# Performance work log

Measured on AMD Instinct MI355X. Metric: run time of the kernel, lower is better.

The kernel has to match this reference:

```python
import jax, jax.numpy as jnp
import numpy as np

N = 100000      # nodes
E = 800000      # edges (avg degree 8)
D_IN = 256      # input feature dim
D_H = 256       # hidden dim (hard-coded in module)
D_OUT = 128     # h_feats


def setup_inputs() -> dict:
    key = jax.random.key(0)
    ks = jax.random.split(key, 8)
    feat = jax.random.normal(ks[0], (N, D_IN), jnp.float32)
    src = jax.random.randint(ks[1], (E,), 0, N, dtype=jnp.int32)
    dst = jax.random.randint(ks[2], (E,), 0, N, dtype=jnp.int32)
    def lin(k, din, dout):
        return jax.random.normal(k, (din, dout), jnp.float32) / np.float32(np.sqrt(din))
    return {
        'feat': feat, 'src': src, 'dst': dst,
        'w_self1': lin(ks[3], D_IN, D_H), 'w_neigh1': lin(ks[4], D_IN, D_H),
        'b1': jnp.zeros((D_H,), jnp.float32),
        'w_self2': lin(ks[5], D_H, D_OUT), 'w_neigh2': lin(ks[6], D_H, D_OUT),
        'b2': jnp.zeros((D_OUT,), jnp.float32),
    }


def _sage_mean(h, src, dst, w_self, w_neigh, b):
    # DGL SAGEConv 'mean': rst = h @ W_self + mean_{in-neighbors}(h) @ W_neigh + b
    ones = jnp.ones((src.shape[0],), h.dtype)
    deg = jax.ops.segment_sum(ones, dst, num_segments=N)          # in-degree per node
    msum = jax.ops.segment_sum(h[src], dst, num_segments=N)      # [N, d] gather-scatter
    mean = msum / jnp.maximum(deg, 1.0)[:, None]                  # zero-degree -> 0
    return h @ w_self + mean @ w_neigh + b


def reference(feat, src, dst, w_self1, w_neigh1, b1, w_self2, w_neigh2, b2):
    h = jax.nn.relu(_sage_mean(feat, src, dst, w_self1, w_neigh1, b1))
    h = jax.nn.relu(_sage_mean(h, src, dst, w_self2, w_neigh2, b2))
    # F.normalize(h, dim=1): x / max(||x||_2, eps)
    norm = jnp.linalg.norm(h, axis=1, keepdims=True)
    return h / jnp.maximum(norm, 1e-12)
```

## Files before the change

kernel.cpp:

```cpp
#include <hip/hip_runtime.h>

#define DIN 256
#define DH  256
#define DOUT 128

typedef __attribute__((ext_vector_type(8))) short bf16x8;
typedef __attribute__((ext_vector_type(4))) float f32x4;
typedef __attribute__((ext_vector_type(2))) float f32x2;
typedef __attribute__((ext_vector_type(4))) unsigned short ushort4v;
typedef __attribute__((ext_vector_type(8))) unsigned short ushort8v;
typedef __attribute__((ext_vector_type(4))) unsigned int uint4v;

static __device__ __forceinline__ unsigned short f2bf(float x) {
    unsigned u = __float_as_uint(x);
    u += 0x7fffu + ((u >> 16) & 1u);
    return (unsigned short)(u >> 16);
}
static __device__ __forceinline__ float bf2f(unsigned short h) {
    return __uint_as_float(((unsigned)h) << 16);
}

static __device__ __forceinline__ void gload16(const unsigned short* g, void* l) {
    __builtin_amdgcn_global_load_lds(
        (const __attribute__((address_space(1))) unsigned int*)g,
        (__attribute__((address_space(3))) unsigned int*)l,
        16, 0, 0);
}

__global__ void count_kernel(const int* __restrict__ dst, int* __restrict__ cnt, int E) {
    int e = blockIdx.x * 256 + threadIdx.x;
    if (e < E) atomicAdd(&cnt[dst[e]], 1);
}

__global__ void block_sums_kernel(const int* __restrict__ cnt, int* __restrict__ partial, int N) {
    __shared__ int sdata[256];
    int t = threadIdx.x;
    int base = blockIdx.x * 1024;
    int s = 0;
#pragma unroll
    for (int j = 0; j < 4; ++j) {
        int i = base + t * 4 + j;
        if (i < N) s += cnt[i];
    }
    sdata[t] = s; __syncthreads();
    for (int o = 128; o; o >>= 1) {
        if (t < o) sdata[t] += sdata[t + o];
        __syncthreads();
    }
    if (t == 0) partial[blockIdx.x] = sdata[0];
}

__global__ void scan_block_kernel(int* __restrict__ cnt, const int* __restrict__ partial,
                                  int* __restrict__ off, int N, int E, int nb) {
    __shared__ int sdata[256];
    __shared__ int pbase;
    int b = blockIdx.x, t = threadIdx.x;

    int pv = (t < nb) ? partial[t] : 0;
    sdata[t] = pv; __syncthreads();
    for (int o = 1; o < 256; o <<= 1) {
        int y = (t >= o) ? sdata[t - o] : 0;
        __syncthreads();
        sdata[t] += y;
        __syncthreads();
    }
    if (t == 0) pbase = (b == 0) ? 0 : sdata[b - 1];
    __syncthreads();
    int base0 = pbase;
    __syncthreads();

    int base = b * 1024;
    int vals[4]; int local = 0;
#pragma unroll
    for (int j = 0; j < 4; ++j) {
        int i = base + t * 4 + j;
        vals[j] = (i < N) ? cnt[i] : 0;
        local += vals[j];
    }
    sdata[t] = local; __syncthreads();
    for (int o = 1; o < 256; o <<= 1) {
        int y = (t >= o) ? sdata[t - o] : 0;
        __syncthreads();
        sdata[t] += y;
        __syncthreads();
    }
    int run = sdata[t] - local + base0;
#pragma unroll
    for (int j = 0; j < 4; ++j) {
        int i = base + t * 4 + j;
        if (i < N) { off[i] = run; cnt[i] = run; }
        run += vals[j];
    }
    if (b == 0 && t == 0) off[N] = E;
}

__global__ void fillprep_kernel(const int* __restrict__ src, const int* __restrict__ dst,
                                int* __restrict__ cursor, int* __restrict__ csr, int E,
                                const float* __restrict__ feat, unsigned short* __restrict__ featb,
                                unsigned int* __restrict__ feat8, long long ncHalf,
                                const float* __restrict__ w_self1, const float* __restrict__ w_neigh1,
                                const float* __restrict__ w_self2, const float* __restrict__ w_neigh2,
                                unsigned short* __restrict__ ws1t, unsigned short* __restrict__ wn1t,
                                unsigned short* __restrict__ wcat,
                                int bFill, int bWt) {
    int b = blockIdx.x;
    if (b < bFill) {
        int e = b * 256 + threadIdx.x;
        if (e < E) {
            int d = dst[e];
            int p = atomicAdd(&cursor[d], 1);
            csr[p] = src[e];
        }
    } else if (b < bFill + bWt) {
        int idx = (b - bFill) * 256 + threadIdx.x;
        if (idx < 65536) {
            int nn = idx >> 8, k = idx & 255;
            ws1t[idx] = f2bf(w_self1[k * 256 + nn]);
        } else if (idx < 131072) {
            int j = idx - 65536; int nn = j >> 8, k = j & 255;
            wn1t[j] = f2bf(w_neigh1[k * 256 + nn]);
        } else if (idx < 163840) {
            int j = idx - 131072; int nn = j >> 8, k = j & 255;
            wcat[j] = f2bf(w_neigh2[k * 128 + nn]);
        } else if (idx < 196608) {
            int j = idx - 163840; int nn = j >> 8, k = j & 255;
            wcat[32768 + j] = f2bf(w_self2[k * 128 + nn]);
        }
    } else {
        long long i = (b - bFill - bWt) * 256LL + threadIdx.x;
        if (i >= ncHalf) return;
        long long i2 = i + ncHalf;
        f32x4 v0 = __builtin_nontemporal_load((const f32x4*)feat + i);
        f32x4 v1 = __builtin_nontemporal_load((const f32x4*)feat + i2);
        ushort4v o0, o1;
        o0[0] = f2bf(v0[0]); o0[1] = f2bf(v0[1]); o0[2] = f2bf(v0[2]); o0[3] = f2bf(v0[3]);
        o1[0] = f2bf(v1[0]); o1[1] = f2bf(v1[1]); o1[2] = f2bf(v1[2]); o1[3] = f2bf(v1[3]);
        *((ushort4v*)featb + i)  = o0;
        *((ushort4v*)featb + i2) = o1;
        int u0 = __builtin_amdgcn_cvt_pk_fp8_f32(v0[0], v0[1], 0, 0);
        u0     = __builtin_amdgcn_cvt_pk_fp8_f32(v0[2], v0[3], u0, 1);
        int u1 = __builtin_amdgcn_cvt_pk_fp8_f32(v1[0], v1[1], 0, 0);
        u1     = __builtin_amdgcn_cvt_pk_fp8_f32(v1[2], v1[3], u1, 1);
        feat8[i]  = (unsigned)u0;
        feat8[i2] = (unsigned)u1;
    }
}

__global__ void gather_mean256_kernel(const unsigned int* __restrict__ feat8, const int* __restrict__ off,
                                      const int* __restrict__ csr, unsigned short* __restrict__ agg, int N) {
    int wid  = (int)((blockIdx.x * (long long)blockDim.x + threadIdx.x) >> 6);
    int lane = threadIdx.x & 63;
    if (wid >= N) return;
    int start = off[wid], end = off[wid + 1];
    const int g   = lane >> 4;
    const int cl  = lane & 15;
    float a[16] = {};
    int e = start;
    for (; e + 7 < end; e += 8) {
        int s0 = csr[e + g], s1 = csr[e + 4 + g];
        uint4v v0 = *(const uint4v*)(feat8 + (long long)s0 * 64 + cl * 4);
        uint4v v1 = *(const uint4v*)(feat8 + (long long)s1 * 64 + cl * 4);
#pragma unroll
        for (int d = 0; d < 4; ++d) {
            f32x2 p0 = __builtin_amdgcn_cvt_pk_f32_fp8((int)v0[d], false);
            f32x2 p1 = __builtin_amdgcn_cvt_pk_f32_fp8((int)v0[d], true);
            f32x2 q0 = __builtin_amdgcn_cvt_pk_f32_fp8((int)v1[d], false);
            f32x2 q1 = __builtin_amdgcn_cvt_pk_f32_fp8((int)v1[d], true);
            a[d * 4 + 0] += p0[0] + q0[0];
            a[d * 4 + 1] += p0[1] + q0[1];
            a[d * 4 + 2] += p1[0] + q1[0];
            a[d * 4 + 3] += p1[1] + q1[1];
        }
    }
    for (; e < end; e += 4) {
        int idx = e + g;
        if (idx < end) {
            int s = csr[idx];
            uint4v v = *(const uint4v*)(feat8 + (long long)s * 64 + cl * 4);
#pragma unroll
            for (int d = 0; d < 4; ++d) {
                f32x2 p0 = __builtin_amdgcn_cvt_pk_f32_fp8((int)v[d], false);
                f32x2 p1 = __builtin_amdgcn_cvt_pk_f32_fp8((int)v[d], true);
                a[d * 4 + 0] += p0[0];
                a[d * 4 + 1] += p0[1];
                a[d * 4 + 2] += p1[0];
                a[d * 4 + 3] += p1[1];
            }
        }
    }
#pragma unroll
    for (int j = 0; j < 16; ++j) {
        a[j] += __shfl_xor(a[j], 16);
        a[j] += __shfl_xor(a[j], 32);
    }
    if (g == 0) {
        float inv = 1.0f / (float)max(end - start, 1);
        ushort8v o0, o1;
#pragma unroll
        for (int j = 0; j < 8; ++j) { o0[j] = f2bf(a[j] * inv); o1[j] = f2bf(a[8 + j] * inv); }
        unsigned short* dstp = agg + (long long)wid * 256 + cl * 16;
        *(ushort8v*)dstp       = o0;
        *(ushort8v*)(dstp + 8) = o1;
    }
}

__global__ __launch_bounds__(512)
void gemm1_kernel(const unsigned short* __restrict__ A,  const unsigned short* __restrict__ WT,
                  const unsigned short* __restrict__ A2, const unsigned short* __restrict__ WT2,
                  const float* __restrict__ bias, unsigned short* __restrict__ C, int M)
{
    const int K = 256;
    __shared__ __align__(16) char lds[2][24576];

    const int tid = threadIdx.x;
    const int wid = tid >> 6, lane = tid & 63;
    const int l15 = lane & 15, lg = lane >> 4;
    const int wr = wid >> 2, wc = wid & 3;
    const int row0 = blockIdx.x * 128;

    long long asrc; int adst;
    {
        int c = tid, r = c >> 2, s = c & 3;
        int kc = s ^ ((r >> 1) & 3);
        asrc = (long long)min(row0 + r, M - 1) * K + kc * 8;
        adst = c * 16;
    }
    long long bsrc[2]; int bdst[2];
#pragma unroll
    for (int i = 0; i < 2; ++i) {
        int c = wid * 128 + i * 64 + lane, r = c >> 2, s = c & 3;
        int kc = s ^ ((r >> 1) & 3);
        bsrc[i] = (long long)r * K + kc * 8;
        bdst[i] = 8192 + c * 16;
    }

    const int slot = (lg ^ ((l15 >> 1) & 3)) * 16;
    int aoff[4], boff[4];
#pragma unroll
    for (int m = 0; m < 4; ++m) aoff[m] = (wr * 64 + m * 16 + l15) * 64 + slot;
#pragma unroll
    for (int n = 0; n < 4; ++n) boff[n] = 8192 + (wc * 64 + n * 16 + l15) * 64 + slot;

    f32x4 acc[4][4] = {};

    auto stage = [&](int buf, int t) {
        const unsigned short* Ap = (t >= 8) ? A2 : A;
        const unsigned short* Wp = (t >= 8) ? WT2 : WT;
        int k0 = (t & 7) * 32;
        gload16(Ap + asrc + k0, &lds[buf][adst]);
        gload16(Wp + bsrc[0] + k0, &lds[buf][bdst[0]]);
        gload16(Wp + bsrc[1] + k0, &lds[buf][bdst[1]]);
    };

    stage(0, 0);
    __syncthreads();

    for (int t = 0; t < 16; ++t) {
        const int cur = t & 1;
        if (t + 1 < 16) stage(cur ^ 1, t + 1);
        const char* L = lds[cur];
        bf16x8 af[4], bfr[4];
#pragma unroll
        for (int m = 0; m < 4; ++m) af[m]  = *(const bf16x8*)(L + aoff[m]);
#pragma unroll
        for (int n = 0; n < 4; ++n) bfr[n] = *(const bf16x8*)(L + boff[n]);
#pragma unroll
        for (int m = 0; m < 4; ++m)
#pragma unroll
            for (int n = 0; n < 4; ++n)
                acc[m][n] = __builtin_amdgcn_mfma_f32_16x16x32_bf16(af[m], bfr[n], acc[m][n], 0, 0, 0);
        __syncthreads();
    }

#pragma unroll
    for (int m = 0; m < 4; ++m) {
#pragma unroll
        for (int rr = 0; rr < 4; ++rr) {
            int grow = row0 + wr * 64 + m * 16 + lg * 4 + rr;
            if (grow >= M) continue;
#pragma unroll
            for (int n = 0; n < 4; ++n) {
                int gcol = wc * 64 + n * 16 + l15;
                float v = fmaxf(acc[m][n][rr] + bias[gcol], 0.f);
                C[(long long)grow * 256 + gcol] = f2bf(v);
            }
        }
    }
}

__global__ __launch_bounds__(512)
void gemm23_kernel(const unsigned short* __restrict__ A, const unsigned short* __restrict__ WT,
                   const float* __restrict__ b2,
                   unsigned short* __restrict__ p2, unsigned short* __restrict__ self2, int M)
{
    const int K = 256;
    __shared__ __align__(16) char lds[2][24576];

    const int tid = threadIdx.x;
    const int wid = tid >> 6, lane = tid & 63;
    const int l15 = lane & 15, lg = lane >> 4;
    const int wr = wid >> 2, wc = wid & 3;
    const int row0 = blockIdx.x * 128;

    long long asrc; int adst;
    {
        int c = tid, r = c >> 2, s = c & 3;
        int kc = s ^ ((r >> 1) & 3);
        asrc = (long long)min(row0 + r, M - 1) * K + kc * 8;
        adst = c * 16;
    }
    long long bsrc[2]; int bdst[2];
#pragma unroll
    for (int i = 0; i < 2; ++i) {
        int c = wid * 128 + i * 64 + lane, r = c >> 2, s = c & 3;
        int kc = s ^ ((r >> 1) & 3);
        bsrc[i] = (long long)r * K + kc * 8;
        bdst[i] = 8192 + c * 16;
    }

    const int slot = (lg ^ ((l15 >> 1) & 3)) * 16;
    int aoff[4], boff[4];
#pragma unroll
    for (int m = 0; m < 4; ++m) aoff[m] = (wr * 64 + m * 16 + l15) * 64 + slot;
#pragma unroll
    for (int n = 0; n < 4; ++n) boff[n] = 8192 + (wc * 64 + n * 16 + l15) * 64 + slot;

    f32x4 acc[4][4] = {};

    auto stage = [&](int buf, int t) {
        int k0 = t * 32;
        gload16(A  + asrc + k0, &lds[buf][adst]);
        gload16(WT + bsrc[0] + k0, &lds[buf][bdst[0]]);
        gload16(WT + bsrc[1] + k0, &lds[buf][bdst[1]]);
    };

    stage(0, 0);
    __syncthreads();

    for (int t = 0; t < 8; ++t) {
        const int cur = t & 1;
        if (t + 1 < 8) stage(cur ^ 1, t + 1);
        const char* L = lds[cur];
        bf16x8 af[4], bfr[4];
#pragma unroll
        for (int m = 0; m < 4; ++m) af[m]  = *(const bf16x8*)(L + aoff[m]);
#pragma unroll
        for (int n = 0; n < 4; ++n) bfr[n] = *(const bf16x8*)(L + boff[n]);
#pragma unroll
        for (int m = 0; m < 4; ++m)
#pragma unroll
            for (int n = 0; n < 4; ++n)
                acc[m][n] = __builtin_amdgcn_mfma_f32_16x16x32_bf16(af[m], bfr[n], acc[m][n], 0, 0, 0);
        __syncthreads();
    }

    if (wc < 2) {
#pragma unroll
        for (int m = 0; m < 4; ++m)
#pragma unroll
            for (int rr = 0; rr < 4; ++rr) {
                int grow = row0 + wr * 64 + m * 16 + lg * 4 + rr;
                if (grow >= M) continue;
#pragma unroll
                for (int n = 0; n < 4; ++n) {
                    int col = wc * 64 + n * 16 + l15;
                    p2[(long long)grow * 128 + col] = f2bf(acc[m][n][rr]);
                }
            }
    } else {
        float bv[4];
#pragma unroll
        for (int n = 0; n < 4; ++n) bv[n] = b2[(wc - 2) * 64 + n * 16 + l15];
#pragma unroll
        for (int m = 0; m < 4; ++m)
#pragma unroll
            for (int rr = 0; rr < 4; ++rr) {
                int grow = row0 + wr * 64 + m * 16 + lg * 4 + rr;
                if (grow >= M) continue;
#pragma unroll
                for (int n = 0; n < 4; ++n) {
                    int col = (wc - 2) * 64 + n * 16 + l15;
                    self2[(long long)grow * 128 + col] = f2bf(acc[m][n][rr] + bv[n]);
                }
            }
    }
}

__global__ void gather_final_kernel(const unsigned short* __restrict__ p2, const int* __restrict__ off,
                                    const int* __restrict__ csr, const unsigned short* __restrict__ self2,
                                    float* __restrict__ out, int N) {
    int wid  = (int)((blockIdx.x * (long long)blockDim.x + threadIdx.x) >> 6);
    int lane = threadIdx.x & 63;
    if (wid >= N) return;
    int start = off[wid], end = off[wid + 1];
    const int g  = lane >> 4;
    const int c8 = (lane & 15) * 8;
    float a[8] = {};
    int e = start;
    for (; e + 7 < end; e += 8) {
        int s0 = csr[e + g], s1 = csr[e + 4 + g];
        ushort8v v0 = *(const ushort8v*)(p2 + (long long)s0 * 128 + c8);
        ushort8v v1 = *(const ushort8v*)(p2 + (long long)s1 * 128 + c8);
#pragma unroll
        for (int j = 0; j < 8; ++j) a[j] += bf2f(v0[j]) + bf2f(v1[j]);
    }
    for (; e < end; e += 4) {
        int idx = e + g;
        if (idx < end) {
            int s = csr[idx];
            ushort8v v = *(const ushort8v*)(p2 + (long long)s * 128 + c8);
#pragma unroll
            for (int j = 0; j < 8; ++j) a[j] += bf2f(v[j]);
        }
    }
#pragma unroll
    for (int j = 0; j < 8; ++j) {
        a[j] += __shfl_xor(a[j], 16);
        a[j] += __shfl_xor(a[j], 32);
    }
    float invd = 1.0f / (float)max(end - start, 1);
    ushort8v sv = *(const ushort8v*)(self2 + (long long)wid * 128 + c8);
    float v[8];
    float ss = 0.f;
#pragma unroll
    for (int j = 0; j < 8; ++j) {
        v[j] = fmaxf(bf2f(sv[j]) + a[j] * invd, 0.f);
        ss += v[j] * v[j];
    }
    ss += __shfl_xor(ss, 1);
    ss += __shfl_xor(ss, 2);
    ss += __shfl_xor(ss, 4);
    ss += __shfl_xor(ss, 8);
    float inv = 1.0f / fmaxf(sqrtf(ss), 1e-12f);
    if (g == 0) {
        f32x4 o0 = { v[0] * inv, v[1] * inv, v[2] * inv, v[3] * inv };
        f32x4 o1 = { v[4] * inv, v[5] * inv, v[6] * inv, v[7] * inv };
        float* dstp = out + (long long)wid * 128 + c8;
        __builtin_nontemporal_store(o0, (f32x4*)dstp);
        __builtin_nontemporal_store(o1, (f32x4*)(dstp + 4));
    }
}

extern "C" void kernel_launch(void* const* d_in, const int* in_sizes, int n_in,
                              void* d_out, int out_size, void* d_ws, size_t ws_size,
                              hipStream_t stream) {
    const float* feat     = (const float*)d_in[0];
    const int*   src      = (const int*)  d_in[1];
    const int*   dst      = (const int*)  d_in[2];
    const float* w_self1  = (const float*)d_in[3];
    const float* w_neigh1 = (const float*)d_in[4];
    const float* b1       = (const float*)d_in[5];
    const float* w_self2  = (const float*)d_in[6];
    const float* w_neigh2 = (const float*)d_in[7];
    const float* b2       = (const float*)d_in[8];
    float* out = (float*)d_out;

    const int N = in_sizes[0] / DIN;
    const int E = in_sizes[1];

    char* ws = (char*)d_ws;
    auto a4k = [](size_t x) { return (x + 4095) & ~(size_t)4095; };
    size_t o = 0;
    int* cnt  = (int*)(ws + o); o += a4k((size_t)N * 4);
    int* off  = (int*)(ws + o); o += a4k((size_t)(N + 1) * 4);
    int* part = (int*)(ws + o); o += a4k(1024);
    int* csr  = (int*)(ws + o); o += a4k((size_t)E * 4);
    unsigned short* ws1t = (unsigned short*)(ws + o); o += a4k((size_t)DIN * DH * 2);
    unsigned short* wn1t = (unsigned short*)(ws + o); o += a4k((size_t)DIN * DH * 2);
    unsigned short* wcat = (unsigned short*)(ws + o); o += a4k((size_t)256 * 256 * 2);
    unsigned int*   feat8 = (unsigned int*)(ws + o); o += a4k((size_t)N * DIN);
    unsigned short* featb = (unsigned short*)(ws + o); o += a4k((size_t)N * DIN * 2);
    unsigned short* aggb  = (unsigned short*)(ws + o); o += a4k((size_t)N * DIN * 2);
    unsigned short* h1b   = (unsigned short*)(ws + o); o += a4k((size_t)N * DH * 2);

    unsigned short* p2b    = featb;
    unsigned short* self2b = aggb;

    const int nblk = (N + 1023) / 1024;

    hipMemsetAsync(cnt, 0, (size_t)N * 4, stream);
    count_kernel<<<(E + 255) / 256, 256, 0, stream>>>(dst, cnt, E);
    block_sums_kernel<<<nblk, 256, 0, stream>>>(cnt, part, N);
    scan_block_kernel<<<nblk, 256, 0, stream>>>(cnt, part, off, N, E, nblk);

    long long ncHalf = (long long)N * DIN / 8;
    const int bFill = (E + 255) / 256;
    const int bWt   = 768;
    const int bCvt  = (int)((ncHalf + 255) / 256);
    fillprep_kernel<<<bFill + bWt + bCvt, 256, 0, stream>>>(
        src, dst, cnt, csr, E,
        feat, featb, feat8, ncHalf,
        w_self1, w_neigh1, w_self2, w_neigh2, ws1t, wn1t, wcat,
        bFill, bWt);

    const int mblk = (N + 127) / 128;

    gather_mean256_kernel<<<(N + 3) / 4, 256, 0, stream>>>(feat8, off, csr, aggb, N);
    gemm1_kernel<<<mblk, 512, 0, stream>>>(featb, ws1t, aggb, wn1t, b1, h1b, N);

    gemm23_kernel<<<mblk, 512, 0, stream>>>(h1b, wcat, b2, p2b, self2b, N);
    gather_final_kernel<<<(N + 3) / 4, 256, 0, stream>>>(p2b, off, csr, self2b, out, N);
}
```

Baseline: 277.8 us.

## Split feature conversion across count and fill kernels, interleaving blocks with atomics

Moves part of the fp32 to bf16/fp8 feature conversion (7000 blocks) into the degree-count kernel and the rest into the CSR fill kernel. Atomic blocks are interleaved evenly with conversion blocks by index arithmetic, so latency-bound atomics overlap with bandwidth-bound conversion. The aim is to hide the atomic kernels' latency behind streaming work and balance the two launches. The cost is a slightly more complex block mapping and a hard-coded split count.

New measurement: 256.3 us. -7.7%, faster.

```diff
diff --git a/kernel.cpp b/kernel.cpp
--- a/kernel.cpp
+++ b/kernel.cpp
@@ -27,9 +27,82 @@
         16, 0, 0);
 }
 
-__global__ void count_kernel(const int* __restrict__ dst, int* __restrict__ cnt, int E) {
-    int e = blockIdx.x * 256 + threadIdx.x;
-    if (e < E) atomicAdd(&cnt[dst[e]], 1);
+static __device__ __forceinline__ void cvt_unit(const float* __restrict__ feat,
+                                                unsigned short* __restrict__ featb,
+                                                unsigned int* __restrict__ feat8,
+                                                long long i, long long ncHalf) {
+    long long i2 = i + ncHalf;
+    f32x4 v0 = __builtin_nontemporal_load((const f32x4*)feat + i);
+    f32x4 v1 = __builtin_nontemporal_load((const f32x4*)feat + i2);
+    ushort4v o0, o1;
+    o0[0] = f2bf(v0[0]); o0[1] = f2bf(v0[1]); o0[2] = f2bf(v0[2]); o0[3] = f2bf(v0[3]);
+    o1[0] = f2bf(v1[0]); o1[1] = f2bf(v1[1]); o1[2] = f2bf(v1[2]); o1[3] = f2bf(v1[3]);
+    *((ushort4v*)featb + i)  = o0;
+    *((ushort4v*)featb + i2) = o1;
+    int u0 = __builtin_amdgcn_cvt_pk_fp8_f32(v0[0], v0[1], 0, 0);
+    u0     = __builtin_amdgcn_cvt_pk_fp8_f32(v0[2], v0[3], u0, 1);
+    int u1 = __builtin_amdgcn_cvt_pk_fp8_f32(v1[0], v1[1], 0, 0);
+    u1     = __builtin_amdgcn_cvt_pk_fp8_f32(v1[2], v1[3], u1, 1);
+    feat8[i]  = (unsigned)u0;
+    feat8[i2] = (unsigned)u1;
+}
+
+__global__ void countcvt_kernel(const int* __restrict__ dst, int* __restrict__ cnt, int E, int bCnt,
+                                const float* __restrict__ feat, unsigned short* __restrict__ featb,
+                                unsigned int* __restrict__ feat8, long long ncHalf, int nA) {
+    int b = blockIdx.x;
+    int t0 = (int)((long long)b * bCnt / nA);
+    int t1 = (int)((long long)(b + 1) * bCnt / nA);
+    if (t1 > t0) {
+        int e = t0 * 256 + threadIdx.x;
+        if (e < E) atomicAdd(&cnt[dst[e]], 1);
+    } else {
+        long long i = (long long)(b - t0) * 256 + threadIdx.x;
+        if (i < ncHalf) cvt_unit(feat, featb, feat8, i, ncHalf);
+    }
+}
+
+__global__ void fillcvt_kernel(const int* __restrict__ src, const int* __restrict__ dst,
+                               int* __restrict__ cursor, int* __restrict__ csr, int E, int bFill,
+                               const float* __restrict__ feat, unsigned short* __restrict__ featb,
+                               unsigned int* __restrict__ feat8, long long ncHalf,
+                               int cvtOff, int bCvtB,
+                               const float* __restrict__ w_self1, const float* __restrict__ w_neigh1,
+                               const float* __restrict__ w_self2, const float* __restrict__ w_neigh2,
+                               unsigned short* __restrict__ ws1t, unsigned short* __restrict__ wn1t,
+                               unsigned short* __restrict__ wcat, int nB) {
+    int b = blockIdx.x;
+    int t0 = (int)((long long)b * bFill / nB);
+    int t1 = (int)((long long)(b + 1) * bFill / nB);
+    if (t1 > t0) {
+        int e = t0 * 256 + threadIdx.x;
+        if (e < E) {
+            int d = dst[e];
+            int p = atomicAdd(&cursor[d], 1);
+            csr[p] = src[e];
+        }
+    } else {
+        int j = b - t0;
+        if (j < bCvtB) {
+            long long i = (long long)(cvtOff + j) * 256 + threadIdx.x;
+            if (i < ncHalf) cvt_unit(feat, featb, feat8, i, ncHalf);
+        } else {
+            int idx = (j - bCvtB) * 256 + threadIdx.x;
+            if (idx < 65536) {
+                int nn = idx >> 8, k = idx & 255;
+                ws1t[idx] = f2bf(w_self1[k * 256 + nn]);
+            } else if (idx < 131072) {
+                int jj = idx - 65536; int nn = jj >> 8, k = jj & 255;
+                wn1t[jj] = f2bf(w_neigh1[k * 256 + nn]);
+            } else if (idx < 163840) {
+                int jj = idx - 131072; int nn = jj >> 8, k = jj & 255;
+                wcat[jj] = f2bf(w_neigh2[k * 128 + nn]);
+            } else if (idx < 196608) {
+                int jj = idx - 163840; int nn = jj >> 8, k = jj & 255;
+                wcat[32768 + jj] = f2bf(w_self2[k * 128 + nn]);
+            }
+        }
+    }
 }
 
 __global__ void block_sums_kernel(const int* __restrict__ cnt, int* __restrict__ partial, int N) {
@@ -92,58 +165,6 @@
         run += vals[j];
     }
     if (b == 0 && t == 0) off[N] = E;
-}
-
-__global__ void fillprep_kernel(const int* __restrict__ src, const int* __restrict__ dst,
-                                int* __restrict__ cursor, int* __restrict__ csr, int E,
-                                const float* __restrict__ feat, unsigned short* __restrict__ featb,
-                                unsigned int* __restrict__ feat8, long long ncHalf,
-                                const float* __restrict__ w_self1, const float* __restrict__ w_neigh1,
-                                const float* __restrict__ w_self2, const float* __restrict__ w_neigh2,
-                                unsigned short* __restrict__ ws1t, unsigned short* __restrict__ wn1t,
-                                unsigned short* __restrict__ wcat,
-                                int bFill, int bWt) {
-    int b = blockIdx.x;
-    if (b < bFill) {
-        int e = b * 256 + threadIdx.x;
-        if (e < E) {
-            int d = dst[e];
-            int p = atomicAdd(&cursor[d], 1);
-            csr[p] = src[e];
-        }
-    } else if (b < bFill + bWt) {
-        int idx = (b - bFill) * 256 + threadIdx.x;
-        if (idx < 65536) {
-            int nn = idx >> 8, k = idx & 255;
-            ws1t[idx] = f2bf(w_self1[k * 256 + nn]);
-        } else if (idx < 131072) {
-            int j = idx - 65536; int nn = j >> 8, k = j & 255;
-            wn1t[j] = f2bf(w_neigh1[k * 256 + nn]);
-        } else if (idx < 163840) {
-            int j = idx - 131072; int nn = j >> 8, k = j & 255;
-            wcat[j] = f2bf(w_neigh2[k * 128 + nn]);
-        } else if (idx < 196608) {
-            int j = idx - 163840; int nn = j >> 8, k = j & 255;
-            wcat[32768 + j] = f2bf(w_self2[k * 128 + nn]);
-        }
-    } else {
-        long long i = (b - bFill - bWt) * 256LL + threadIdx.x;
-        if (i >= ncHalf) return;
-        long long i2 = i + ncHalf;
-        f32x4 v0 = __builtin_nontemporal_load((const f32x4*)feat + i);
-        f32x4 v1 = __builtin_nontemporal_load((const f32x4*)feat + i2);
-        ushort4v o0, o1;
-        o0[0] = f2bf(v0[0]); o0[1] = f2bf(v0[1]); o0[2] = f2bf(v0[2]); o0[3] = f2bf(v0[3]);
-        o1[0] = f2bf(v1[0]); o1[1] = f2bf(v1[1]); o1[2] = f2bf(v1[2]); o1[3] = f2bf(v1[3]);
-        *((ushort4v*)featb + i)  = o0;
-        *((ushort4v*)featb + i2) = o1;
-        int u0 = __builtin_amdgcn_cvt_pk_fp8_f32(v0[0], v0[1], 0, 0);
-        u0     = __builtin_amdgcn_cvt_pk_fp8_f32(v0[2], v0[3], u0, 1);
-        int u1 = __builtin_amdgcn_cvt_pk_fp8_f32(v1[0], v1[1], 0, 0);
-        u1     = __builtin_amdgcn_cvt_pk_fp8_f32(v1[2], v1[3], u1, 1);
-        feat8[i]  = (unsigned)u0;
-        feat8[i2] = (unsigned)u1;
-    }
 }
 
 __global__ void gather_mean256_kernel(const unsigned int* __restrict__ feat8, const int* __restrict__ off,
@@ -478,20 +499,25 @@
 
     const int nblk = (N + 1023) / 1024;
 
+    long long ncHalf = (long long)N * DIN / 8;
+    const int bCvtTot = (int)((ncHalf + 255) / 256);
+    const int bCvtA = 7000;
+    const int bCvtB = bCvtTot - bCvtA;
+    const int bAtom = (E + 255) / 256;
+    const int bWt   = 768;
+
     hipMemsetAsync(cnt, 0, (size_t)N * 4, stream);
-    count_kernel<<<(E + 255) / 256, 256, 0, stream>>>(dst, cnt, E);
+    const int nA = bCvtA + bAtom;
+    countcvt_kernel<<<nA, 256, 0, stream>>>(dst, cnt, E, bAtom, feat, featb, feat8, ncHalf, nA);
+
     block_sums_kernel<<<nblk, 256, 0, stream>>>(cnt, part, N);
     scan_block_kernel<<<nblk, 256, 0, stream>>>(cnt, part, off, N, E, nblk);
 
-    long long ncHalf = (long long)N * DIN / 8;
-    const int bFill = (E + 255) / 256;
-    const int bWt   = 768;
-    const int bCvt  = (int)((ncHalf + 255) / 256);
-    fillprep_kernel<<<bFill + bWt + bCvt, 256, 0, stream>>>(
-        src, dst, cnt, csr, E,
-        feat, featb, feat8, ncHalf,
-        w_self1, w_neigh1, w_self2, w_neigh2, ws1t, wn1t, wcat,
-        bFill, bWt);
+    const int nB = bCvtB + bWt + bAtom;
+    fillcvt_kernel<<<nB, 256, 0, stream>>>(
+        src, dst, cnt, csr, E, bAtom,
+        feat, featb, feat8, ncHalf, bCvtA, bCvtB,
+        w_self1, w_neigh1, w_self2, w_neigh2, ws1t, wn1t, wcat, nB);
 
     const int mblk = (N + 127) / 128;
 
```
